# Performance work log

Measured on AMD Instinct MI355X. Metric: run time of the kernel, lower is better.

The kernel has to match this reference:

```python
import jax, jax.numpy as jnp
import numpy as np
import math

HIDDEN = 1024
HEADS = 16
HEAD_DIM = HIDDEN // HEADS
B, S = 2, 2048


def _xavier(key, shape):
    fan_in, fan_out = shape[1], shape[0]
    limit = math.sqrt(6.0 / (fan_in + fan_out))
    return jax.random.uniform(key, shape, jnp.float32, -limit, limit)


def setup_inputs() -> dict:
    key = jax.random.key(0)
    ks = jax.random.split(key, 5)
    x = jax.random.normal(ks[0], (B, S, HIDDEN), jnp.float32)
    # torch Linear stores weight as [out, in]; y = x @ W.T + b
    Wq = _xavier(ks[1], (HIDDEN, HIDDEN))
    Wk = _xavier(ks[2], (HIDDEN, HIDDEN))
    Wv = _xavier(ks[3], (HIDDEN, HIDDEN))
    Wo = _xavier(ks[4], (HIDDEN, HIDDEN))
    bq = jnp.zeros((HIDDEN,), jnp.float32)
    bk = jnp.zeros((HIDDEN,), jnp.float32)
    bv = jnp.zeros((HIDDEN,), jnp.float32)
    bo = jnp.zeros((HIDDEN,), jnp.float32)
    return {"x": x, "Wq": Wq, "bq": bq, "Wk": Wk, "bk": bk,
            "Wv": Wv, "bv": bv, "Wo": Wo, "bo": bo}


def reference(x, Wq, bq, Wk, bk, Wv, bv, Wo, bo):
    b, s, d = x.shape
    h, hd = HEADS, HEAD_DIM
    q = (x @ Wq.T + bq).reshape(b, s, h, hd).transpose(0, 2, 1, 3)  # [b,h,s,hd]
    k = (x @ Wk.T + bk).reshape(b, s, h, hd).transpose(0, 2, 1, 3)
    v = (x @ Wv.T + bv).reshape(b, s, h, hd).transpose(0, 2, 1, 3)
    scores = jnp.einsum('bhqd,bhkd->bhqk', q, k) / math.sqrt(hd)
    causal = jnp.tril(jnp.ones((s, s), bool))
    scores = jnp.where(causal, scores, -jnp.inf)
    attn = jax.nn.softmax(scores, axis=-1)
    out = jnp.einsum('bhqk,bhkd->bhqd', attn, v)  # [b,h,s,hd]
    out = out.transpose(0, 2, 1, 3).reshape(b, s, d)
    return out @ Wo.T + bo
```

## Files before the change

kernel.cpp:

```cpp
#include <hip/hip_runtime.h>
#include <hip/hip_bf16.h>


typedef __hip_bfloat16 bf16;
typedef __attribute__((ext_vector_type(8))) short short8;
typedef __attribute__((ext_vector_type(4))) short short4v;
typedef __attribute__((ext_vector_type(4))) float f32x4;
typedef __attribute__((ext_vector_type(2))) unsigned uint2v;
typedef __attribute__((ext_vector_type(4))) unsigned uint4v;

#define MFMA16(a, b, c) __builtin_amdgcn_mfma_f32_16x16x32_bf16((a), (b), (c), 0, 0, 0)

__device__ __forceinline__ void load_lds16(const void* g, void* l) {
  __builtin_amdgcn_global_load_lds(
      (const __attribute__((address_space(1))) void*)g,
      (__attribute__((address_space(3))) void*)l, 16, 0, 0);
}

#define QSCALE 0.18033688f

__global__ __launch_bounds__(256) void cvt_kernel(
    const float* __restrict__ x, const float* __restrict__ wq,
    const float* __restrict__ wk, const float* __restrict__ wv,
    const float* __restrict__ wo, bf16* __restrict__ xb,
    bf16* __restrict__ wcat) {
  const int bx = blockIdx.x;
  const float* src;
  bf16* dst;
  int ib;
  if (bx < 4096) { src = x; dst = xb; ib = bx; }
  else {
    const int wseg = (bx - 4096) >> 10;
    ib = (bx - 4096) & 1023;
    src = wseg == 0 ? wq : wseg == 1 ? wk : wseg == 2 ? wv : wo;
    dst = wcat + (size_t)wseg * 1048576;
  }
  const int i = (ib * 256 + threadIdx.x) * 4;
  const float4 v = *(const float4*)(src + i);
  short4v p;
  *(__hip_bfloat162*)&p = __float22bfloat162_rn(float2{v.x, v.y});
  *((__hip_bfloat162*)&p + 1) = __float22bfloat162_rn(float2{v.z, v.w});
  *(short4v*)(dst + i) = p;
}

__global__ __launch_bounds__(256) void qkv_kernel(
    const bf16* __restrict__ x, const bf16* __restrict__ Wcat,
    const float* __restrict__ bq, const float* __restrict__ bk,
    const float* __restrict__ bv, bf16* __restrict__ Qb,
    bf16* __restrict__ Kb, bf16* __restrict__ Vtg) {
  constexpr int K = 1024;
  __shared__ bf16 As[128 * 64];
  __shared__ bf16 Bs[128 * 64];
  const int t = threadIdx.x;
  const int lane = t & 63, w = t >> 6;
  const int quad = lane >> 4, r = lane & 15;
  const int m0 = blockIdx.y * 128;
  const int ncol = blockIdx.x * 128;
  const int seg = ncol >> 10;
  const int n0 = ncol & 1023;
  const int wm = w >> 1, wn = w & 1;

  f32x4 acc[4][4] = {};

  for (int k0 = 0; k0 < K; k0 += 64) {
    __syncthreads();
#pragma unroll
    for (int p = 0; p < 4; ++p) {
      const int c = p * 256 + w * 64 + lane;
      const int row = c >> 3;
      const int scb = (c & 7) ^ (row & 7);
      load_lds16(x + (size_t)(m0 + row) * K + k0 + scb * 8, As + c * 8);
    }
#pragma unroll
    for (int p = 0; p < 4; ++p) {
      const int c = p * 256 + w * 64 + lane;
      const int row = c >> 3;
      const int scb = (c & 7) ^ (row & 7);
      load_lds16(Wcat + (size_t)(ncol + row) * K + k0 + scb * 8, Bs + c * 8);
    }
    __syncthreads();
    short8 af[4][2], bfr[4][2];
#pragma unroll
    for (int ks = 0; ks < 2; ++ks) {
#pragma unroll
      for (int i = 0; i < 4; ++i) {
        const int ra = wm * 64 + i * 16 + r;
        af[i][ks] = *(const short8*)(As + ra * 64 +
                                     (((ks * 4 + quad) ^ (ra & 7)) * 8));
        const int rb = wn * 64 + i * 16 + r;
        bfr[i][ks] = *(const short8*)(Bs + rb * 64 +
                                      (((ks * 4 + quad) ^ (rb & 7)) * 8));
      }
    }
#pragma unroll
    for (int ks = 0; ks < 2; ++ks)
#pragma unroll
      for (int i = 0; i < 4; ++i)
#pragma unroll
        for (int j = 0; j < 4; ++j)
          acc[i][j] = MFMA16(af[i][ks], bfr[j][ks], acc[i][j]);
  }

  const float* bias = seg == 0 ? bq : seg == 1 ? bk : bv;
  const float scale = seg == 0 ? QSCALE : 1.0f;
  bf16* dst01 = seg == 0 ? Qb : Kb;
#pragma unroll
  for (int i = 0; i < 4; ++i) {
    const int m = m0 + wm * 64 + i * 16 + quad * 4;
#pragma unroll
    for (int j = 0; j < 4; ++j) {
      const int nn = n0 + wn * 64 + j * 16 + r;
      const float bv_ = bias[nn];
      if (seg == 2) {
        short4v pk;
        *(__hip_bfloat162*)&pk = __float22bfloat162_rn(
            float2{acc[i][j][0] + bv_, acc[i][j][1] + bv_});
        *((__hip_bfloat162*)&pk + 1) = __float22bfloat162_rn(
            float2{acc[i][j][2] + bv_, acc[i][j][3] + bv_});
        *(short4v*)(Vtg + (size_t)nn * 4096 + m) = pk;
      } else {
#pragma unroll
        for (int g = 0; g < 4; ++g)
          dst01[(size_t)(m + g) * 1024 + nn] =
              __float2bfloat16((acc[i][j][g] + bv_) * scale);
      }
    }
  }
}

__global__ __launch_bounds__(256) void proj_kernel(const bf16* __restrict__ X,
                                                   const bf16* __restrict__ W,
                                                   const float* __restrict__ bias,
                                                   float* __restrict__ Y) {
  constexpr int K = 1024, N = 1024;
  __shared__ bf16 As[64 * 64];
  __shared__ bf16 Bs[128 * 64];
  const int t = threadIdx.x;
  const int lane = t & 63, w = t >> 6;
  const int quad = lane >> 4, r = lane & 15;
  const int m0 = blockIdx.y * 64, n0 = blockIdx.x * 128;
  const int wm = w >> 1, wn = w & 1;

  f32x4 acc[2][4] = {};

  for (int k0 = 0; k0 < K; k0 += 64) {
    __syncthreads();
#pragma unroll
    for (int p = 0; p < 2; ++p) {
      const int c = p * 256 + w * 64 + lane;
      const int row = c >> 3;
      const int scb = (c & 7) ^ (row & 7);
      load_lds16(X + (size_t)(m0 + row) * K + k0 + scb * 8, As + c * 8);
    }
#pragma unroll
    for (int p = 0; p < 4; ++p) {
      const int c = p * 256 + w * 64 + lane;
      const int row = c >> 3;
      const int scb = (c & 7) ^ (row & 7);
      load_lds16(W + (size_t)(n0 + row) * K + k0 + scb * 8, Bs + c * 8);
    }
    __syncthreads();
    short8 af[2][2], bfr[4][2];
#pragma unroll
    for (int ks = 0; ks < 2; ++ks) {
#pragma unroll
      for (int i = 0; i < 2; ++i) {
        const int ra = wm * 32 + i * 16 + r;
        af[i][ks] = *(const short8*)(As + ra * 64 +
                                     (((ks * 4 + quad) ^ (ra & 7)) * 8));
      }
#pragma unroll
      for (int j = 0; j < 4; ++j) {
        const int rb = wn * 64 + j * 16 + r;
        bfr[j][ks] = *(const short8*)(Bs + rb * 64 +
                                      (((ks * 4 + quad) ^ (rb & 7)) * 8));
      }
    }
#pragma unroll
    for (int ks = 0; ks < 2; ++ks)
#pragma unroll
      for (int i = 0; i < 2; ++i)
#pragma unroll
        for (int j = 0; j < 4; ++j)
          acc[i][j] = MFMA16(af[i][ks], bfr[j][ks], acc[i][j]);
  }
#pragma unroll
  for (int i = 0; i < 2; ++i) {
    const int m = m0 + wm * 32 + i * 16 + quad * 4;
#pragma unroll
    for (int j = 0; j < 4; ++j) {
      const int n = n0 + wn * 64 + j * 16 + r;
      const float bv = bias[n];
#pragma unroll
      for (int g = 0; g < 4; ++g)
        Y[(size_t)(m + g) * N + n] = acc[i][j][g] + bv;
    }
  }
}

__global__ __launch_bounds__(512, 8) void attn_kernel(const bf16* __restrict__ Qb,
                                                      const bf16* __restrict__ Kb,
                                                      const bf16* __restrict__ Vtg,
                                                      bf16* __restrict__ Ob) {
  const int n = blockIdx.x;
  const int gl = n & 7, pair = (n >> 3) & 15, gh = n >> 7;
  const int g = gl + 8 * gh;
  const int h = g & 15, b = g >> 4;
  const int t = threadIdx.x;
  const int lane = t & 63, w = t >> 6;
  const int qs = w >> 1, kst = w & 1;
  const int quad = lane >> 4, r = lane & 15;

  __shared__ __align__(16) bf16 smem[16384];
  bf16* const ks_base = smem;
  bf16* const vt_base = smem + 8192;

  const int c = t;
  const int row = c >> 3, scb = (c & 7) ^ (row & 7);
  const bf16* const kg = Kb + (size_t)(b * 2048 + row) * 1024 + h * 64 + scb * 8;
  const bf16* const vg = Vtg + (size_t)(h * 64 + row) * 4096 +
                         (size_t)b * 2048 + scb * 8;
  const int c8 = c * 8;

  auto stage_tile = [&](int tile, int buf) {
    load_lds16(kg + (size_t)tile * 65536, ks_base + buf * 4096 + c8);
    load_lds16(vg + tile * 64,            vt_base + buf * 4096 + c8);
  };

  auto pass = [&](const int j, const int nt) {
    const int qrow = j * 64 + qs * 16 + r;

    short8 qf[2];
#pragma unroll
    for (int ks = 0; ks < 2; ++ks)
      qf[ks] = *(const short8*)(Qb + (size_t)(b * 2048 + qrow) * 1024 +
                                h * 64 + ks * 32 + quad * 8);

    f32x4 o[4] = {};
    float lsum = 0.f;

    stage_tile(0, 0);
    for (int s = 0; s < nt; ++s) {
      if (s + 1 < nt) {
        stage_tile(s + 1, (s + 1) & 1);
        asm volatile("s_waitcnt vmcnt(2)" ::: "memory");
      } else {
        asm volatile("s_waitcnt vmcnt(0)" ::: "memory");
      }
      __builtin_amdgcn_s_barrier();
      __builtin_amdgcn_sched_barrier(0);

      const bf16* const ksb = ks_base + (s & 1) * 4096;
      const bf16* const vtb = vt_base + (s & 1) * 4096;

      short8 kf[2][2];
#pragma unroll
      for (int mt = 0; mt < 2; ++mt) {
        const int krow = kst * 32 + mt * 16 + r;
#pragma unroll
        for (int ks = 0; ks < 2; ++ks)
          kf[mt][ks] = *(const short8*)(ksb + krow * 64 +
                                        (((ks * 4 + quad) ^ (r & 7)) * 8));
      }
      f32x4 st[2] = {};
#pragma unroll
      for (int mt = 0; mt < 2; ++mt) {
        st[mt] = MFMA16(kf[mt][0], qf[0], st[mt]);
        st[mt] = MFMA16(kf[mt][1], qf[1], st[mt]);
      }
      if (s == nt - 1) {
#pragma unroll
        for (int mt = 0; mt < 2; ++mt) {
          const int kb = s * 64 + kst * 32 + mt * 16 + quad * 4;
#pragma unroll
          for (int g4 = 0; g4 < 4; ++g4)
            if (kb + g4 > qrow) st[mt][g4] = -1e30f;
        }
      }
      unsigned cpk[2][2];
#pragma unroll
      for (int mt = 0; mt < 2; ++mt) {
        const float p0 = exp2f(st[mt][0]), p1 = exp2f(st[mt][1]);
        const float p2 = exp2f(st[mt][2]), p3 = exp2f(st[mt][3]);
        lsum += (p0 + p1) + (p2 + p3);
        unsigned u0, u1;
        *(__hip_bfloat162*)&u0 = __float22bfloat162_rn(float2{p0, p1});
        *(__hip_bfloat162*)&u1 = __float22bfloat162_rn(float2{p2, p3});
        cpk[mt][0] = u0;
        cpk[mt][1] = u1;
      }
      unsigned br[4];
#pragma unroll
      for (int p = 0; p < 2; ++p) {
        uint2v s32 = __builtin_amdgcn_permlane32_swap(cpk[0][p], cpk[1][p],
                                                      false, false);
        uint2v s16 = __builtin_amdgcn_permlane16_swap(s32.x, s32.y,
                                                      false, false);
        br[p] = s16.x; br[p + 2] = s16.y;
      }
      uint4v pv_; pv_.x = br[0]; pv_.y = br[1]; pv_.z = br[2]; pv_.w = br[3];
      const short8 pf = __builtin_bit_cast(short8, pv_);

#pragma unroll
      for (int mt = 0; mt < 4; ++mt) {
        const short8 vf = *(const short8*)(vtb + (mt * 16 + r) * 64 +
                                           (((kst * 4 + quad) ^ (r & 7)) * 8));
        o[mt] = MFMA16(vf, pf, o[mt]);
      }

      __builtin_amdgcn_sched_barrier(0);
      __builtin_amdgcn_s_barrier();
    }

    lsum += __shfl_xor(lsum, 16);
    lsum += __shfl_xor(lsum, 32);
    __syncthreads();
    f32x4* const cb = (f32x4*)smem;
    float* const lb = (float*)(smem + 8192);
    if (kst == 1) {
#pragma unroll
      for (int mt = 0; mt < 4; ++mt) cb[(qs * 4 + mt) * 64 + lane] = o[mt];
      lb[qs * 64 + lane] = lsum;
    }
    __syncthreads();
    if (kst == 0) {
#pragma unroll
      for (int mt = 0; mt < 4; ++mt) {
        const f32x4 a = cb[(qs * 4 + mt) * 64 + lane];
#pragma unroll
        for (int g4 = 0; g4 < 4; ++g4) o[mt][g4] += a[g4];
      }
      const float inv = 1.f / (lsum + lb[qs * 64 + lane]);
#pragma unroll
      for (int mt = 0; mt < 4; ++mt) {
        const int d0 = mt * 16 + quad * 4;
        short4v ph;
        *(__hip_bfloat162*)&ph = __float22bfloat162_rn(
            float2{o[mt][0] * inv, o[mt][1] * inv});
        *((__hip_bfloat162*)&ph + 1) = __float22bfloat162_rn(
            float2{o[mt][2] * inv, o[mt][3] * inv});
        *(short4v*)(Ob + (size_t)(b * 2048 + qrow) * 1024 + h * 64 + d0) = ph;
      }
    }
    __syncthreads();
  };

  pass(31 - pair, 32 - pair);
  pass(pair, pair + 1);
}

extern "C" void kernel_launch(void* const* d_in, const int* in_sizes, int n_in,
                              void* d_out, int out_size, void* d_ws, size_t ws_size,
                              hipStream_t stream) {
  const float* x  = (const float*)d_in[0];
  const float* Wq = (const float*)d_in[1];
  const float* bq = (const float*)d_in[2];
  const float* Wk = (const float*)d_in[3];
  const float* bk = (const float*)d_in[4];
  const float* Wv = (const float*)d_in[5];
  const float* bv = (const float*)d_in[6];
  const float* Wo = (const float*)d_in[7];
  const float* bo = (const float*)d_in[8];
  float* out = (float*)d_out;

  bf16* xb   = (bf16*)d_ws;
  bf16* wcat = xb + (size_t)4096 * 1024;
  bf16* wob  = wcat + (size_t)3 * 1024 * 1024;
  bf16* Qb   = wcat + (size_t)4 * 1024 * 1024;
  bf16* Kb   = Qb  + (size_t)4096 * 1024;
  bf16* Vtg  = Kb  + (size_t)4096 * 1024;
  bf16* Ob   = Vtg + (size_t)4096 * 1024;
  const size_t need = ((size_t)4096 * 1024 * 5 + (size_t)1024 * 1024 * 4) * 2;
  if (ws_size < need) return;

  cvt_kernel<<<8192, 256, 0, stream>>>(x, Wq, Wk, Wv, Wo, xb, wcat);
  qkv_kernel<<<dim3(24, 32), 256, 0, stream>>>(xb, wcat, bq, bk, bv,
                                               Qb, Kb, Vtg);
  attn_kernel<<<512, 512, 0, stream>>>(Qb, Kb, Vtg, Ob);
  proj_kernel<<<dim3(8, 64), 256, 0, stream>>>(Ob, wob, bo, out);
}
```

Baseline: 184.6 us.

## Merge two attention passes into one quad-buffered K/V stream

Replaces the two sequential per-block passes (high and low query tile) with a single loop over all 33 K/V tiles. The loop switches which query fragments and accumulators it uses at the boundary, and it prefetches three tiles ahead into four LDS buffers instead of double buffering. This removes the pipeline drain and refill plus the reduction syncs between passes, and it drops one barrier per iteration. In exchange the block uses twice the LDS (64 KB) and holds two sets of accumulators, so launch bounds drop to 4 blocks per CU and occupancy falls.

```diff
diff --git a/kernel.cpp b/kernel.cpp
--- a/kernel.cpp
+++ b/kernel.cpp
@@ -198,7 +198,7 @@
   }
 }
 
-__global__ __launch_bounds__(512, 8) void attn_kernel(const bf16* __restrict__ Qb,
+__global__ __launch_bounds__(512, 4) void attn_kernel(const bf16* __restrict__ Qb,
                                                       const bf16* __restrict__ Kb,
                                                       const bf16* __restrict__ Vtg,
                                                       bf16* __restrict__ Ob) {
@@ -211,9 +211,16 @@
   const int qs = w >> 1, kst = w & 1;
   const int quad = lane >> 4, r = lane & 15;
 
-  __shared__ __align__(16) bf16 smem[16384];
+  __shared__ __align__(16) bf16 smem[32768];
   bf16* const ks_base = smem;
-  bf16* const vt_base = smem + 8192;
+  bf16* const vt_base = smem + 16384;
+
+  const int T = 32 - pair;
+  const int NL = pair + 1;
+  const int NS = T + NL;
+
+  const int qrow_hi = (31 - pair) * 64 + qs * 16 + r;
+  const int qrow_lo = pair * 64 + qs * 16 + r;
 
   const int c = t;
   const int row = c >> 3, scb = (c & 7) ^ (row & 7);
@@ -227,126 +234,142 @@
     load_lds16(vg + tile * 64,            vt_base + buf * 4096 + c8);
   };
 
-  auto pass = [&](const int j, const int nt) {
-    const int qrow = j * 64 + qs * 16 + r;
-
-    short8 qf[2];
-#pragma unroll
-    for (int ks = 0; ks < 2; ++ks)
-      qf[ks] = *(const short8*)(Qb + (size_t)(b * 2048 + qrow) * 1024 +
-                                h * 64 + ks * 32 + quad * 8);
-
-    f32x4 o[4] = {};
-    float lsum = 0.f;
-
-    stage_tile(0, 0);
-    for (int s = 0; s < nt; ++s) {
-      if (s + 1 < nt) {
-        stage_tile(s + 1, (s + 1) & 1);
-        asm volatile("s_waitcnt vmcnt(2)" ::: "memory");
-      } else {
-        asm volatile("s_waitcnt vmcnt(0)" ::: "memory");
+  short8 qfh[2], qfl[2];
+#pragma unroll
+  for (int ks = 0; ks < 2; ++ks) {
+    qfh[ks] = *(const short8*)(Qb + (size_t)(b * 2048 + qrow_hi) * 1024 +
+                               h * 64 + ks * 32 + quad * 8);
+    qfl[ks] = *(const short8*)(Qb + (size_t)(b * 2048 + qrow_lo) * 1024 +
+                               h * 64 + ks * 32 + quad * 8);
+  }
+
+  f32x4 oh[4] = {}, ol[4] = {};
+  float lsh = 0.f, lsl = 0.f;
+
+  auto compute = [&](const bf16* ksb, const bf16* vtb, const short8* qf,
+                     f32x4 (&o)[4], float& lsum, int ta, int qrow, bool mask) {
+    short8 kf[2][2];
+#pragma unroll
+    for (int mt = 0; mt < 2; ++mt) {
+      const int krow = kst * 32 + mt * 16 + r;
+#pragma unroll
+      for (int ks = 0; ks < 2; ++ks)
+        kf[mt][ks] = *(const short8*)(ksb + krow * 64 +
+                                      (((ks * 4 + quad) ^ (r & 7)) * 8));
+    }
+    f32x4 st[2] = {};
+#pragma unroll
+    for (int mt = 0; mt < 2; ++mt) {
+      st[mt] = MFMA16(kf[mt][0], qf[0], st[mt]);
+      st[mt] = MFMA16(kf[mt][1], qf[1], st[mt]);
+    }
+    if (mask) {
+#pragma unroll
+      for (int mt = 0; mt < 2; ++mt) {
+        const int kb = ta * 64 + kst * 32 + mt * 16 + quad * 4;
+#pragma unroll
+        for (int g4 = 0; g4 < 4; ++g4)
+          if (kb + g4 > qrow) st[mt][g4] = -1e30f;
       }
-      __builtin_amdgcn_s_barrier();
-      __builtin_amdgcn_sched_barrier(0);
-
-      const bf16* const ksb = ks_base + (s & 1) * 4096;
-      const bf16* const vtb = vt_base + (s & 1) * 4096;
-
-      short8 kf[2][2];
-#pragma unroll
-      for (int mt = 0; mt < 2; ++mt) {
-        const int krow = kst * 32 + mt * 16 + r;
-#pragma unroll
-        for (int ks = 0; ks < 2; ++ks)
-          kf[mt][ks] = *(const short8*)(ksb + krow * 64 +
-                                        (((ks * 4 + quad) ^ (r & 7)) * 8));
-      }
-      f32x4 st[2] = {};
-#pragma unroll
-      for (int mt = 0; mt < 2; ++mt) {
-        st[mt] = MFMA16(kf[mt][0], qf[0], st[mt]);
-        st[mt] = MFMA16(kf[mt][1], qf[1], st[mt]);
-      }
-      if (s == nt - 1) {
-#pragma unroll
-        for (int mt = 0; mt < 2; ++mt) {
-          const int kb = s * 64 + kst * 32 + mt * 16 + quad * 4;
-#pragma unroll
-          for (int g4 = 0; g4 < 4; ++g4)
-            if (kb + g4 > qrow) st[mt][g4] = -1e30f;
-        }
-      }
-      unsigned cpk[2][2];
-#pragma unroll
-      for (int mt = 0; mt < 2; ++mt) {
-        const float p0 = exp2f(st[mt][0]), p1 = exp2f(st[mt][1]);
-        const float p2 = exp2f(st[mt][2]), p3 = exp2f(st[mt][3]);
-        lsum += (p0 + p1) + (p2 + p3);
-        unsigned u0, u1;
-        *(__hip_bfloat162*)&u0 = __float22bfloat162_rn(float2{p0, p1});
-        *(__hip_bfloat162*)&u1 = __float22bfloat162_rn(float2{p2, p3});
-        cpk[mt][0] = u0;
-        cpk[mt][1] = u1;
-      }
-      unsigned br[4];
-#pragma unroll
-      for (int p = 0; p < 2; ++p) {
-        uint2v s32 = __builtin_amdgcn_permlane32_swap(cpk[0][p], cpk[1][p],
-                                                      false, false);
-        uint2v s16 = __builtin_amdgcn_permlane16_swap(s32.x, s32.y,
-                                                      false, false);
-        br[p] = s16.x; br[p + 2] = s16.y;
-      }
-      uint4v pv_; pv_.x = br[0]; pv_.y = br[1]; pv_.z = br[2]; pv_.w = br[3];
-      const short8 pf = __builtin_bit_cast(short8, pv_);
-
-#pragma unroll
-      for (int mt = 0; mt < 4; ++mt) {
-        const short8 vf = *(const short8*)(vtb + (mt * 16 + r) * 64 +
-                                           (((kst * 4 + quad) ^ (r & 7)) * 8));
-        o[mt] = MFMA16(vf, pf, o[mt]);
-      }
-
-      __builtin_amdgcn_sched_barrier(0);
-      __builtin_amdgcn_s_barrier();
-    }
-
-    lsum += __shfl_xor(lsum, 16);
-    lsum += __shfl_xor(lsum, 32);
-    __syncthreads();
-    f32x4* const cb = (f32x4*)smem;
-    float* const lb = (float*)(smem + 8192);
-    if (kst == 1) {
-#pragma unroll
-      for (int mt = 0; mt < 4; ++mt) cb[(qs * 4 + mt) * 64 + lane] = o[mt];
-      lb[qs * 64 + lane] = lsum;
-    }
-    __syncthreads();
-    if (kst == 0) {
-#pragma unroll
-      for (int mt = 0; mt < 4; ++mt) {
-        const f32x4 a = cb[(qs * 4 + mt) * 64 + lane];
-#pragma unroll
-        for (int g4 = 0; g4 < 4; ++g4) o[mt][g4] += a[g4];
-      }
-      const float inv = 1.f / (lsum + lb[qs * 64 + lane]);
-#pragma unroll
-      for (int mt = 0; mt < 4; ++mt) {
-        const int d0 = mt * 16 + quad * 4;
-        short4v ph;
-        *(__hip_bfloat162*)&ph = __float22bfloat162_rn(
-            float2{o[mt][0] * inv, o[mt][1] * inv});
-        *((__hip_bfloat162*)&ph + 1) = __float22bfloat162_rn(
-            float2{o[mt][2] * inv, o[mt][3] * inv});
-        *(short4v*)(Ob + (size_t)(b * 2048 + qrow) * 1024 + h * 64 + d0) = ph;
-      }
-    }
-    __syncthreads();
+    }
+    unsigned cpk[2][2];
+#pragma unroll
+    for (int mt = 0; mt < 2; ++mt) {
+      const float p0 = exp2f(st[mt][0]), p1 = exp2f(st[mt][1]);
+      const float p2 = exp2f(st[mt][2]), p3 = exp2f(st[mt][3]);
+      lsum += (p0 + p1) + (p2 + p3);
+      unsigned u0, u1;
+      *(__hip_bfloat162*)&u0 = __float22bfloat162_rn(float2{p0, p1});
+      *(__hip_bfloat162*)&u1 = __float22bfloat162_rn(float2{p2, p3});
+      cpk[mt][0] = u0;
+      cpk[mt][1] = u1;
+    }
+    unsigned br[4];
+#pragma unroll
+    for (int p = 0; p < 2; ++p) {
+      uint2v s32 = __builtin_amdgcn_permlane32_swap(cpk[0][p], cpk[1][p],
+                                                    false, false);
+      uint2v s16 = __builtin_amdgcn_permlane16_swap(s32.x, s32.y,
+                                                    false, false);
+      br[p] = s16.x; br[p + 2] = s16.y;
+    }
+    uint4v pv_; pv_.x = br[0]; pv_.y = br[1]; pv_.z = br[2]; pv_.w = br[3];
+    const short8 pf = __builtin_bit_cast(short8, pv_);
+
+#pragma unroll
+    for (int mt = 0; mt < 4; ++mt) {
+      const short8 vf = *(const short8*)(vtb + (mt * 16 + r) * 64 +
+                                         (((kst * 4 + quad) ^ (r & 7)) * 8));
+      o[mt] = MFMA16(vf, pf, o[mt]);
+    }
   };
 
-  pass(31 - pair, 32 - pair);
-  pass(pair, pair + 1);
+  stage_tile(0, 0);
+  stage_tile(1, 1);
+  stage_tile(2, 2);
+
+  for (int s = 0; s < NS; ++s) {
+    __builtin_amdgcn_s_barrier();
+    if (s + 3 < NS) {
+      const int sn = s + 3;
+      stage_tile(sn < T ? sn : sn - T, sn & 3);
+    }
+    const int fl = NS - 1 - s;
+    if (fl >= 3)      asm volatile("s_waitcnt vmcnt(6)" ::: "memory");
+    else if (fl == 2) asm volatile("s_waitcnt vmcnt(4)" ::: "memory");
+    else if (fl == 1) asm volatile("s_waitcnt vmcnt(2)" ::: "memory");
+    else              asm volatile("s_waitcnt vmcnt(0)" ::: "memory");
+    __builtin_amdgcn_sched_barrier(0);
+
+    const bf16* const ksb = ks_base + (s & 3) * 4096;
+    const bf16* const vtb = vt_base + (s & 3) * 4096;
+    if (s < T) compute(ksb, vtb, qfh, oh, lsh, s, qrow_hi, s == T - 1);
+    else       compute(ksb, vtb, qfl, ol, lsl, s - T, qrow_lo, s == NS - 1);
+  }
+
+  lsh += __shfl_xor(lsh, 16);
+  lsh += __shfl_xor(lsh, 32);
+  lsl += __shfl_xor(lsl, 16);
+  lsl += __shfl_xor(lsl, 32);
+  __syncthreads();
+  f32x4* const cb = (f32x4*)smem;
+  float* const lb = (float*)(smem + 16384);
+  if (kst == 1) {
+#pragma unroll
+    for (int mt = 0; mt < 4; ++mt) {
+      cb[((qs * 2 + 0) * 4 + mt) * 64 + lane] = oh[mt];
+      cb[((qs * 2 + 1) * 4 + mt) * 64 + lane] = ol[mt];
+    }
+    lb[(qs * 2 + 0) * 64 + lane] = lsh;
+    lb[(qs * 2 + 1) * 64 + lane] = lsl;
+  }
+  __syncthreads();
+  if (kst == 0) {
+#pragma unroll
+    for (int mt = 0; mt < 4; ++mt) {
+      const f32x4 ah = cb[((qs * 2 + 0) * 4 + mt) * 64 + lane];
+      const f32x4 al = cb[((qs * 2 + 1) * 4 + mt) * 64 + lane];
+#pragma unroll
+      for (int g4 = 0; g4 < 4; ++g4) { oh[mt][g4] += ah[g4]; ol[mt][g4] += al[g4]; }
+    }
+    const float invh = 1.f / (lsh + lb[(qs * 2 + 0) * 64 + lane]);
+    const float invl = 1.f / (lsl + lb[(qs * 2 + 1) * 64 + lane]);
+#pragma unroll
+    for (int mt = 0; mt < 4; ++mt) {
+      const int d0 = mt * 16 + quad * 4;
+      short4v ph, pl2;
+      *(__hip_bfloat162*)&ph = __float22bfloat162_rn(
+          float2{oh[mt][0] * invh, oh[mt][1] * invh});
+      *((__hip_bfloat162*)&ph + 1) = __float22bfloat162_rn(
+          float2{oh[mt][2] * invh, oh[mt][3] * invh});
+      *(short4v*)(Ob + (size_t)(b * 2048 + qrow_hi) * 1024 + h * 64 + d0) = ph;
+      *(__hip_bfloat162*)&pl2 = __float22bfloat162_rn(
+          float2{ol[mt][0] * invl, ol[mt][1] * invl});
+      *((__hip_bfloat162*)&pl2 + 1) = __float22bfloat162_rn(
+          float2{ol[mt][2] * invl, ol[mt][3] * invl});
+      *(short4v*)(Ob + (size_t)(b * 2048 + qrow_lo) * 1024 + h * 64 + d0) = pl2;
+    }
+  }
 }
 
 extern "C" void kernel_launch(void* const* d_in, const int* in_sizes, int n_in,
```

New measurement: 180.6 us. -2.2%, faster.

## Restructure attention into 256-thread blocks with two key tiles per step

Applied to the files above, without the earlier changes.

The attention kernel drops to 4 waves per block. Each wave now owns 32 query rows and 64 keys, and the two key-tile groups each take a whole 64-key tile, so every step processes two tiles at once. The two causal passes are merged into a single pipelined loop that prefetches the next pair of tiles while computing on the current pair, and the exp and priority hints are tuned. This raises MFMA work per LDS fragment load and halves the number of barrier steps, at the cost of more registers per wave and a larger LDS footprint.

```diff
diff --git a/kernel.cpp b/kernel.cpp
--- a/kernel.cpp
+++ b/kernel.cpp
@@ -198,7 +198,7 @@
   }
 }
 
-__global__ __launch_bounds__(512, 8) void attn_kernel(const bf16* __restrict__ Qb,
+__global__ __launch_bounds__(256, 2) void attn_kernel(const bf16* __restrict__ Qb,
                                                       const bf16* __restrict__ Kb,
                                                       const bf16* __restrict__ Vtg,
                                                       bf16* __restrict__ Ob) {
@@ -208,145 +208,215 @@
   const int h = g & 15, b = g >> 4;
   const int t = threadIdx.x;
   const int lane = t & 63, w = t >> 6;
-  const int qs = w >> 1, kst = w & 1;
+  const int ktg = w >> 1, qs = w & 1;
   const int quad = lane >> 4, r = lane & 15;
 
-  __shared__ __align__(16) bf16 smem[16384];
-  bf16* const ks_base = smem;
-  bf16* const vt_base = smem + 8192;
+  __shared__ __align__(16) bf16 smem[32768];
+
+  const int T = 32 - pair, NL = pair + 1;
+  const int sh = (T + 1) >> 1;
+  const int NSTEP = sh + ((NL + 1) >> 1);
+  const int jhi = 31 - pair, jlo = pair;
 
   const int c = t;
-  const int row = c >> 3, scb = (c & 7) ^ (row & 7);
-  const bf16* const kg = Kb + (size_t)(b * 2048 + row) * 1024 + h * 64 + scb * 8;
-  const bf16* const vg = Vtg + (size_t)(h * 64 + row) * 4096 +
-                         (size_t)b * 2048 + scb * 8;
+  const int srow = c >> 3, scb = (c & 7) ^ (srow & 7);
+  const bf16* const kg0 = Kb + (size_t)(b * 2048 + srow) * 1024 + h * 64 + scb * 8;
+  const bf16* const vg0 = Vtg + (size_t)(h * 64 + srow) * 4096 +
+                          (size_t)b * 2048 + scb * 8;
   const int c8 = c * 8;
 
-  auto stage_tile = [&](int tile, int buf) {
-    load_lds16(kg + (size_t)tile * 65536, ks_base + buf * 4096 + c8);
-    load_lds16(vg + tile * 64,            vt_base + buf * 4096 + c8);
+  auto stage_tile = [&](int tile, int slot) {
+    bf16* const kd = smem + slot * 4096;
+    bf16* const vd = smem + 16384 + slot * 4096;
+    const bf16* const ksrc = kg0 + (size_t)tile * 65536;
+    const bf16* const vsrc = vg0 + tile * 64;
+    load_lds16(ksrc, kd + c8);
+    load_lds16(ksrc + 32 * 1024, kd + c8 + 2048);
+    load_lds16(vsrc, vd + c8);
+    load_lds16(vsrc + (size_t)32 * 4096, vd + c8 + 2048);
   };
 
-  auto pass = [&](const int j, const int nt) {
-    const int qrow = j * 64 + qs * 16 + r;
-
-    short8 qf[2];
-#pragma unroll
-    for (int ks = 0; ks < 2; ++ks)
-      qf[ks] = *(const short8*)(Qb + (size_t)(b * 2048 + qrow) * 1024 +
-                                h * 64 + ks * 32 + quad * 8);
-
-    f32x4 o[4] = {};
-    float lsum = 0.f;
-
-    stage_tile(0, 0);
-    for (int s = 0; s < nt; ++s) {
-      if (s + 1 < nt) {
-        stage_tile(s + 1, (s + 1) & 1);
-        asm volatile("s_waitcnt vmcnt(2)" ::: "memory");
-      } else {
-        asm volatile("s_waitcnt vmcnt(0)" ::: "memory");
-      }
-      __builtin_amdgcn_s_barrier();
-      __builtin_amdgcn_sched_barrier(0);
-
-      const bf16* const ksb = ks_base + (s & 1) * 4096;
-      const bf16* const vtb = vt_base + (s & 1) * 4096;
-
-      short8 kf[2][2];
-#pragma unroll
-      for (int mt = 0; mt < 2; ++mt) {
-        const int krow = kst * 32 + mt * 16 + r;
-#pragma unroll
-        for (int ks = 0; ks < 2; ++ks)
-          kf[mt][ks] = *(const short8*)(ksb + krow * 64 +
-                                        (((ks * 4 + quad) ^ (r & 7)) * 8));
-      }
-      f32x4 st[2] = {};
-#pragma unroll
-      for (int mt = 0; mt < 2; ++mt) {
-        st[mt] = MFMA16(kf[mt][0], qf[0], st[mt]);
-        st[mt] = MFMA16(kf[mt][1], qf[1], st[mt]);
-      }
-      if (s == nt - 1) {
-#pragma unroll
-        for (int mt = 0; mt < 2; ++mt) {
-          const int kb = s * 64 + kst * 32 + mt * 16 + quad * 4;
+  const int eA = r * 64 + ((quad ^ (r & 7)) * 8);
+  const int eB = r * 64 + (((4 + quad) ^ (r & 7)) * 8);
+
+  short8 qf[2][2];
+  auto load_q = [&](int j) {
+#pragma unroll
+    for (int qfr = 0; qfr < 2; ++qfr)
+#pragma unroll
+      for (int ks = 0; ks < 2; ++ks)
+        qf[qfr][ks] = *(const short8*)(
+            Qb + (size_t)(b * 2048 + j * 64 + qs * 32 + qfr * 16 + r) * 1024 +
+            h * 64 + ks * 32 + quad * 8);
+  };
+
+  const f32x4 fzero = {};
+  f32x4 o[4][2] = {};
+  float lsum[2] = {0.f, 0.f};
+
+  auto compute = [&](int slot, int tt, int Tph, int j) {
+    const bf16* const kb_ = smem + slot * 4096;
+    const bf16* const vb_ = smem + 16384 + slot * 4096;
+    short8 kf[4][2];
+#pragma unroll
+    for (int mt = 0; mt < 4; ++mt) {
+      kf[mt][0] = *(const short8*)(kb_ + mt * 1024 + eA);
+      kf[mt][1] = *(const short8*)(kb_ + mt * 1024 + eB);
+    }
+    f32x4 st[4][2] = {};
+#pragma unroll
+    for (int mt = 0; mt < 4; ++mt)
+#pragma unroll
+      for (int qfr = 0; qfr < 2; ++qfr) {
+        st[mt][qfr] = MFMA16(kf[mt][0], qf[qfr][0], st[mt][qfr]);
+        st[mt][qfr] = MFMA16(kf[mt][1], qf[qfr][1], st[mt][qfr]);
+      }
+    if (tt == Tph - 1) {
+#pragma unroll
+      for (int mt = 0; mt < 4; ++mt)
+#pragma unroll
+        for (int qfr = 0; qfr < 2; ++qfr) {
+          const int kb2 = tt * 64 + mt * 16 + quad * 4;
+          const int qrow = j * 64 + qs * 32 + qfr * 16 + r;
 #pragma unroll
           for (int g4 = 0; g4 < 4; ++g4)
-            if (kb + g4 > qrow) st[mt][g4] = -1e30f;
+            if (kb2 + g4 > qrow) st[mt][qfr][g4] = -1e30f;
         }
-      }
-      unsigned cpk[2][2];
-#pragma unroll
-      for (int mt = 0; mt < 2; ++mt) {
-        const float p0 = exp2f(st[mt][0]), p1 = exp2f(st[mt][1]);
-        const float p2 = exp2f(st[mt][2]), p3 = exp2f(st[mt][3]);
-        lsum += (p0 + p1) + (p2 + p3);
+    }
+    unsigned cpk[4][2][2];
+#pragma unroll
+    for (int mt = 0; mt < 4; ++mt)
+#pragma unroll
+      for (int qfr = 0; qfr < 2; ++qfr) {
+        const float p0 = __builtin_amdgcn_exp2f(st[mt][qfr][0]);
+        const float p1 = __builtin_amdgcn_exp2f(st[mt][qfr][1]);
+        const float p2 = __builtin_amdgcn_exp2f(st[mt][qfr][2]);
+        const float p3 = __builtin_amdgcn_exp2f(st[mt][qfr][3]);
+        lsum[qfr] += (p0 + p1) + (p2 + p3);
         unsigned u0, u1;
         *(__hip_bfloat162*)&u0 = __float22bfloat162_rn(float2{p0, p1});
         *(__hip_bfloat162*)&u1 = __float22bfloat162_rn(float2{p2, p3});
-        cpk[mt][0] = u0;
-        cpk[mt][1] = u1;
-      }
-      unsigned br[4];
-#pragma unroll
-      for (int p = 0; p < 2; ++p) {
-        uint2v s32 = __builtin_amdgcn_permlane32_swap(cpk[0][p], cpk[1][p],
-                                                      false, false);
-        uint2v s16 = __builtin_amdgcn_permlane16_swap(s32.x, s32.y,
-                                                      false, false);
-        br[p] = s16.x; br[p + 2] = s16.y;
-      }
-      uint4v pv_; pv_.x = br[0]; pv_.y = br[1]; pv_.z = br[2]; pv_.w = br[3];
-      const short8 pf = __builtin_bit_cast(short8, pv_);
-
-#pragma unroll
-      for (int mt = 0; mt < 4; ++mt) {
-        const short8 vf = *(const short8*)(vtb + (mt * 16 + r) * 64 +
-                                           (((kst * 4 + quad) ^ (r & 7)) * 8));
-        o[mt] = MFMA16(vf, pf, o[mt]);
-      }
-
-      __builtin_amdgcn_sched_barrier(0);
-      __builtin_amdgcn_s_barrier();
-    }
-
-    lsum += __shfl_xor(lsum, 16);
-    lsum += __shfl_xor(lsum, 32);
-    __syncthreads();
-    f32x4* const cb = (f32x4*)smem;
-    float* const lb = (float*)(smem + 8192);
-    if (kst == 1) {
-#pragma unroll
-      for (int mt = 0; mt < 4; ++mt) cb[(qs * 4 + mt) * 64 + lane] = o[mt];
-      lb[qs * 64 + lane] = lsum;
-    }
-    __syncthreads();
-    if (kst == 0) {
-#pragma unroll
-      for (int mt = 0; mt < 4; ++mt) {
-        const f32x4 a = cb[(qs * 4 + mt) * 64 + lane];
-#pragma unroll
-        for (int g4 = 0; g4 < 4; ++g4) o[mt][g4] += a[g4];
-      }
-      const float inv = 1.f / (lsum + lb[qs * 64 + lane]);
-#pragma unroll
-      for (int mt = 0; mt < 4; ++mt) {
-        const int d0 = mt * 16 + quad * 4;
-        short4v ph;
-        *(__hip_bfloat162*)&ph = __float22bfloat162_rn(
-            float2{o[mt][0] * inv, o[mt][1] * inv});
-        *((__hip_bfloat162*)&ph + 1) = __float22bfloat162_rn(
-            float2{o[mt][2] * inv, o[mt][3] * inv});
-        *(short4v*)(Ob + (size_t)(b * 2048 + qrow) * 1024 + h * 64 + d0) = ph;
-      }
-    }
-    __syncthreads();
+        cpk[mt][qfr][0] = u0;
+        cpk[mt][qfr][1] = u1;
+      }
+    short8 pf[2][2];
+#pragma unroll
+    for (int kk = 0; kk < 2; ++kk)
+#pragma unroll
+      for (int qfr = 0; qfr < 2; ++qfr) {
+        unsigned br[4];
+#pragma unroll
+        for (int p2 = 0; p2 < 2; ++p2) {
+          uint2v s32 = __builtin_amdgcn_permlane32_swap(
+              cpk[kk * 2][qfr][p2], cpk[kk * 2 + 1][qfr][p2], false, false);
+          uint2v s16 = __builtin_amdgcn_permlane16_swap(s32.x, s32.y,
+                                                        false, false);
+          br[p2] = s16.x; br[p2 + 2] = s16.y;
+        }
+        uint4v pv_; pv_.x = br[0]; pv_.y = br[1]; pv_.z = br[2]; pv_.w = br[3];
+        pf[kk][qfr] = __builtin_bit_cast(short8, pv_);
+      }
+#pragma unroll
+    for (int mt = 0; mt < 4; ++mt) {
+      const short8 vf0 = *(const short8*)(vb_ + mt * 1024 + eA);
+      const short8 vf1 = *(const short8*)(vb_ + mt * 1024 + eB);
+#pragma unroll
+      for (int qfr = 0; qfr < 2; ++qfr) {
+        o[mt][qfr] = MFMA16(vf0, pf[0][qfr], o[mt][qfr]);
+        o[mt][qfr] = MFMA16(vf1, pf[1][qfr], o[mt][qfr]);
+      }
+    }
   };
 
-  pass(31 - pair, 32 - pair);
-  pass(pair, pair + 1);
+  auto combine_store = [&](int j, int dp) {
+#pragma unroll
+    for (int qfr = 0; qfr < 2; ++qfr) {
+      lsum[qfr] += __shfl_xor(lsum[qfr], 16);
+      lsum[qfr] += __shfl_xor(lsum[qfr], 32);
+    }
+    f32x4* const cb = (f32x4*)((char*)smem + dp * 16384);
+    float* const lb = (float*)((char*)smem + 32768 + dp * 16384);
+    if (ktg == 1) {
+#pragma unroll
+      for (int mt = 0; mt < 4; ++mt)
+#pragma unroll
+        for (int qfr = 0; qfr < 2; ++qfr)
+          cb[((qs * 4 + mt) * 2 + qfr) * 64 + lane] = o[mt][qfr];
+#pragma unroll
+      for (int qfr = 0; qfr < 2; ++qfr)
+        lb[(qs * 2 + qfr) * 64 + lane] = lsum[qfr];
+    }
+    __syncthreads();
+    if (ktg == 0) {
+      float inv[2];
+#pragma unroll
+      for (int qfr = 0; qfr < 2; ++qfr)
+        inv[qfr] = 1.f / (lsum[qfr] + lb[(qs * 2 + qfr) * 64 + lane]);
+#pragma unroll
+      for (int mt = 0; mt < 4; ++mt)
+#pragma unroll
+        for (int qfr = 0; qfr < 2; ++qfr) {
+          const f32x4 a = cb[((qs * 4 + mt) * 2 + qfr) * 64 + lane];
+          short4v ph;
+          *(__hip_bfloat162*)&ph = __float22bfloat162_rn(
+              float2{(o[mt][qfr][0] + a[0]) * inv[qfr],
+                     (o[mt][qfr][1] + a[1]) * inv[qfr]});
+          *((__hip_bfloat162*)&ph + 1) = __float22bfloat162_rn(
+              float2{(o[mt][qfr][2] + a[2]) * inv[qfr],
+                     (o[mt][qfr][3] + a[3]) * inv[qfr]});
+          *(short4v*)(Ob +
+              (size_t)(b * 2048 + j * 64 + qs * 32 + qfr * 16 + r) * 1024 +
+              h * 64 + mt * 16 + quad * 4) = ph;
+        }
+    }
+    __syncthreads();
+  };
+
+  load_q(jhi);
+  stage_tile(0, 0);
+  stage_tile(1, 1);
+
+  for (int s = 0; s < NSTEP; ++s) {
+    if (s == sh) {
+      combine_store(jhi, (sh - 1) & 1);
+#pragma unroll
+      for (int mt = 0; mt < 4; ++mt)
+#pragma unroll
+        for (int qfr = 0; qfr < 2; ++qfr) o[mt][qfr] = fzero;
+      lsum[0] = lsum[1] = 0.f;
+      load_q(jlo);
+    }
+    const int sx = s + 1;
+    if (sx < NSTEP) {
+      int t0, t1;
+      if (sx < sh) { t0 = 2 * sx; t1 = 2 * sx + 1; if (t1 >= T) t1 = t0; }
+      else { const int lx = sx - sh; t0 = 2 * lx; t1 = 2 * lx + 1;
+             if (t1 >= NL) t1 = t0; }
+      const int p1 = sx & 1;
+      stage_tile(t0, p1 * 2);
+      stage_tile(t1, p1 * 2 + 1);
+      asm volatile("s_waitcnt vmcnt(8)" ::: "memory");
+    } else {
+      asm volatile("s_waitcnt vmcnt(0)" ::: "memory");
+    }
+    __builtin_amdgcn_s_barrier();
+    __builtin_amdgcn_sched_barrier(0);
+
+    const int p = s & 1;
+    __builtin_amdgcn_s_setprio(1);
+    if (s < sh) {
+      const int tt = 2 * s + ktg;
+      if (tt < T) compute(p * 2 + ktg, tt, T, jhi);
+    } else {
+      const int tt = 2 * (s - sh) + ktg;
+      if (tt < NL) compute(p * 2 + ktg, tt, NL, jlo);
+    }
+    __builtin_amdgcn_s_setprio(0);
+    __builtin_amdgcn_sched_barrier(0);
+    __builtin_amdgcn_s_barrier();
+  }
+
+  combine_store(jlo, 1);
 }
 
 extern "C" void kernel_launch(void* const* d_in, const int* in_sizes, int n_in,
@@ -376,6 +446,6 @@
   cvt_kernel<<<8192, 256, 0, stream>>>(x, Wq, Wk, Wv, Wo, xb, wcat);
   qkv_kernel<<<dim3(24, 32), 256, 0, stream>>>(xb, wcat, bq, bk, bv,
                                                Qb, Kb, Vtg);
-  attn_kernel<<<512, 512, 0, stream>>>(Qb, Kb, Vtg, Ob);
+  attn_kernel<<<512, 256, 0, stream>>>(Qb, Kb, Vtg, Ob);
   proj_kernel<<<dim3(8, 64), 256, 0, stream>>>(Ob, wob, bo, out);
 }
```

Result: faster. 177.1 us (-4.1%).
